# Optimization experiments

Measured on AMD Instinct MI355X. Metric: run time of the kernel, lower is better.

Reference implementation:

```python
import jax, jax.numpy as jnp
import numpy as np

GROUPS = 8
EPS = 1e-5

def setup_inputs() -> dict:
    key = jax.random.key(0)
    ks = jax.random.split(key, 5)
    B, C, H, W = 4, 256, 64, 64
    x = jax.random.normal(ks[0], (B, C, H, W), dtype=jnp.float32)
    gn_weight = jnp.ones((C,), dtype=jnp.float32)
    gn_bias = jnp.zeros((C,), dtype=jnp.float32)
    qkv_w = jax.random.normal(ks[1], (3 * C, C), dtype=jnp.float32) * (1.0 / np.sqrt(C))
    qkv_b = jax.random.normal(ks[2], (3 * C,), dtype=jnp.float32) * 0.02
    proj_w = jax.random.normal(ks[3], (C, C), dtype=jnp.float32) * (1.0 / np.sqrt(C))
    proj_b = jax.random.normal(ks[4], (C,), dtype=jnp.float32) * 0.02
    return {"x": x, "gn_weight": gn_weight, "gn_bias": gn_bias,
            "qkv_w": qkv_w, "qkv_b": qkv_b, "proj_w": proj_w, "proj_b": proj_b}

def _group_norm(x, weight, bias):
    B, C, H, W = x.shape
    xg = x.reshape(B, GROUPS, C // GROUPS, H, W)
    mean = jnp.mean(xg, axis=(2, 3, 4), keepdims=True)
    var = jnp.var(xg, axis=(2, 3, 4), keepdims=True)
    xn = ((xg - mean) * jax.lax.rsqrt(var + EPS)).reshape(B, C, H, W)
    return xn * weight[None, :, None, None] + bias[None, :, None, None]

def reference(x, gn_weight, gn_bias, qkv_w, qkv_b, proj_w, proj_b):
    B, C, H, W = x.shape
    N = H * W
    h = _group_norm(x, gn_weight, gn_bias)            # [B,C,H,W]
    hf = h.reshape(B, C, N)                           # [B,C,N]
    # 1x1 conv == channel matmul
    qkv = jnp.einsum('oc,bcn->bon', qkv_w, hf) + qkv_b[None, :, None]  # [B,3C,N]
    q, k, v = jnp.split(qkv, 3, axis=1)               # each [B,C,N]
    scale = 1.0 / jnp.sqrt(jnp.float32(C))
    attn = jax.nn.softmax(jnp.einsum('bcn,bcm->bnm', q, k) * scale, axis=-1)  # [B,N,N]
    o = jnp.einsum('bnm,bcm->bcn', attn, v)           # [B,C,N]
    o = jnp.einsum('oc,bcn->bon', proj_w, o) + proj_b[None, :, None]
    return x + o.reshape(B, C, H, W)
```

## Files before the change

### kernel.cpp

```cpp
#include <hip/hip_runtime.h>
#include <math.h>


#define BATCH 4
#define CH 256
#define NSP 4096
#define NGRP 8
#define CPG 32

typedef __attribute__((ext_vector_type(8))) short bf16x8;
typedef __attribute__((ext_vector_type(4))) float f32x4;

__device__ __forceinline__ unsigned short f2bf(float f) {
  union { float f; unsigned u; } v; v.f = f;
  unsigned r = v.u + 0x7FFF + ((v.u >> 16) & 1);
  return (unsigned short)(r >> 16);
}

__device__ __forceinline__ void gload_lds16(const void* g, void* l) {
  __builtin_amdgcn_global_load_lds(
      (const __attribute__((address_space(1))) unsigned int*)g,
      (__attribute__((address_space(3))) unsigned int*)l, 16, 0, 0);
}

__global__ __launch_bounds__(256) void gn_part_k(const float* __restrict__ x,
                                                 float* __restrict__ gpart) {
  const int bid = blockIdx.x;
  const int bg = bid >> 3, sl = bid & 7;
  const float4* p = (const float4*)(x + (size_t)bg * CPG * NSP + (size_t)sl * (CPG * NSP / 8));
  const int t = threadIdx.x;
  float s1 = 0.f, s2 = 0.f;
#pragma unroll
  for (int i = 0; i < 16; ++i) {
    float4 v = p[t + i * 256];
    s1 += v.x + v.y + v.z + v.w;
    s2 += v.x * v.x + v.y * v.y + v.z * v.z + v.w * v.w;
  }
  __shared__ float r1[256], r2[256];
  r1[t] = s1; r2[t] = s2;
  __syncthreads();
  for (int off = 128; off > 0; off >>= 1) {
    if (t < off) { r1[t] += r1[t + off]; r2[t] += r2[t + off]; }
    __syncthreads();
  }
  if (t == 0) { gpart[bid * 2] = r1[0]; gpart[bid * 2 + 1] = r2[0]; }
}

__global__ __launch_bounds__(256) void fold_k(const float* __restrict__ gn_w,
                                              const float* __restrict__ gn_b,
                                              const float* __restrict__ qkv_w,
                                              const float* __restrict__ qkv_b,
                                              const float* __restrict__ proj_w,
                                              const float* __restrict__ gpart,
                                              float* __restrict__ ascale,
                                              float* __restrict__ bias2,
                                              unsigned short* __restrict__ wb,
                                              unsigned short* __restrict__ pwb) {
  const int b = blockIdx.x;
  const int t = threadIdx.x;
  __shared__ float bb[CH];
  {
    const int c = t;
    const int g = c >> 5;
    float s1 = 0.f, s2 = 0.f;
#pragma unroll
    for (int s = 0; s < 8; ++s) {
      s1 += gpart[((b * NGRP + g) * 8 + s) * 2];
      s2 += gpart[((b * NGRP + g) * 8 + s) * 2 + 1];
    }
    const float inv = 1.f / (float)(CPG * NSP);
    const float mean = s1 * inv;
    const float var = s2 * inv - mean * mean;
    const float rstd = rsqrtf(var + 1e-5f);
    const float a = rstd * gn_w[c];
    ascale[b * CH + c] = a;
    bb[c] = gn_b[c] - mean * a;
  }
  __syncthreads();
  for (int o = t; o < 3 * CH; o += 256) {
    const float* wrow = qkv_w + (size_t)o * CH;
    float acc = qkv_b[o];
    for (int c = 0; c < CH; ++c) acc += wrow[c] * bb[c];
    if (o < CH) acc *= 0.0625f;
    bias2[b * 3 * CH + o] = acc;
  }
  for (int idx = t; idx < 192 * CH; idx += 256) {
    const int row = b * 192 + (idx >> 8);
    const int c = idx & 255;
    float w = qkv_w[(size_t)row * CH + c];
    if (row < CH) w *= 0.0625f;
    wb[(size_t)row * CH + c] = f2bf(w);
  }
  for (int idx = t; idx < 64 * CH; idx += 256) {
    const int row = b * 64 + (idx >> 8);
    const int c = idx & 255;
    pwb[(size_t)row * CH + c] = f2bf(proj_w[(size_t)row * CH + c]);
  }
}

__global__ __launch_bounds__(256) void xt_k(const float* __restrict__ x,
                                            const float* __restrict__ ascale,
                                            unsigned short* __restrict__ xbT) {
  const int b = blockIdx.z, cb = blockIdx.y * 64, nb = blockIdx.x * 64;
  const int t = threadIdx.x;
  __shared__ float Ls[64][68];
  for (int i = 0; i < 4; ++i) {
    const int idx = t + i * 256;
    const int c = idx >> 4, n4 = (idx & 15) << 2;
    const float a = ascale[b * CH + cb + c];
    const float4 v = *(const float4*)(x + ((size_t)(b * CH + cb + c)) * NSP + nb + n4);
    Ls[c][n4] = v.x * a; Ls[c][n4 + 1] = v.y * a;
    Ls[c][n4 + 2] = v.z * a; Ls[c][n4 + 3] = v.w * a;
  }
  __syncthreads();
  {
    const int n = t >> 2, cg = (t & 3) << 4;
    unsigned int pk[8];
#pragma unroll
    for (int j = 0; j < 8; ++j) {
      const unsigned short l16 = f2bf(Ls[cg + 2 * j][n]);
      const unsigned short h16 = f2bf(Ls[cg + 2 * j + 1][n]);
      pk[j] = (unsigned)l16 | ((unsigned)h16 << 16);
    }
    unsigned short* dst = xbT + ((size_t)(b * NSP) + nb + n) * CH + cb + cg;
    *(uint4*)dst = *(uint4*)&pk[0];
    *(uint4*)(dst + 8) = *(uint4*)&pk[4];
  }
}

__global__ __launch_bounds__(256) void qkv_mfma_k(const unsigned short* __restrict__ wb,
                                                  const unsigned short* __restrict__ xbT,
                                                  const float* __restrict__ bias2,
                                                  unsigned short* __restrict__ qT,
                                                  unsigned short* __restrict__ kT,
                                                  unsigned short* __restrict__ vN) {
  const int b = blockIdx.z, ob = blockIdx.y * 64, nb = blockIdx.x * 64;
  const int t = threadIdx.x;
  __shared__ short Ws[64][264];
  __shared__ short Xs[64][264];
  for (int i = 0; i < 8; ++i) {
    const int idx = t + i * 256;
    const int row = idx >> 5, u = (idx & 31) << 3;
    *(float4*)&Ws[row][u] = *(const float4*)(wb + ((size_t)(ob + row)) * CH + u);
    *(float4*)&Xs[row][u] = *(const float4*)(xbT + ((size_t)(b * NSP) + nb + row) * CH + u);
  }
  __syncthreads();
  const int lane = t & 63, wave = t >> 6, lo = lane & 15, hi = lane >> 4;
  const f32x4 zero = {0.f, 0.f, 0.f, 0.f};
  f32x4 acc[4] = {zero, zero, zero, zero};
#pragma unroll
  for (int ks = 0; ks < 8; ++ks) {
    const bf16x8 a = *(const bf16x8*)&Ws[wave * 16 + lo][ks * 32 + hi * 8];
#pragma unroll
    for (int nt = 0; nt < 4; ++nt) {
      const bf16x8 xv = *(const bf16x8*)&Xs[nt * 16 + lo][ks * 32 + hi * 8];
      acc[nt] = __builtin_amdgcn_mfma_f32_16x16x32_bf16(a, xv, acc[nt], 0, 0, 0);
    }
  }
#pragma unroll
  for (int nt = 0; nt < 4; ++nt) {
#pragma unroll
    for (int r = 0; r < 4; ++r) {
      const int o = ob + wave * 16 + hi * 4 + r;
      const int n = nb + nt * 16 + lo;
      const float v = acc[nt][r] + bias2[b * 3 * CH + o];
      if (o < CH)            qT[((size_t)(b * NSP) + n) * CH + o] = f2bf(v);
      else if (o < 2 * CH)   kT[((size_t)(b * NSP) + n) * CH + (o - CH)] = f2bf(v);
      else                   vN[((size_t)(b * CH) + (o - 2 * CH)) * NSP + n] = f2bf(v);
    }
  }
}

__global__ __launch_bounds__(512, 2) void attn_mfma_k(const unsigned short* __restrict__ qT,
                                                      const unsigned short* __restrict__ kT,
                                                      const unsigned short* __restrict__ vN,
                                                      unsigned short* __restrict__ oTb) {
  const int bid = blockIdx.x;
  const int L = (bid & 7) * 32 + (bid >> 3);
  const int b = L >> 6;
  const int qb = (L & 63) * 64;

  const int t = threadIdx.x;
  const int wid = t >> 6, lane = t & 63, lo = lane & 15, hi = lane >> 4;
  const int pair = wid >> 1, wip = wid & 1;

  __shared__ __align__(16) char smem[142336];
  short* Psw = (short*)(smem + 131072) + wid * 16 * 40;
  float* sM = (float*)(smem + 141312);
  float* sL = sM + 128;

  const unsigned short* kTb = kT + (size_t)b * NSP * CH;
  const unsigned short* vNb = vN + (size_t)b * CH * NSP;

  const int qrow = qb + pair * 16 + lo;
  bf16x8 qreg[8];
#pragma unroll
  for (int ks = 0; ks < 8; ++ks)
    qreg[ks] = *(const bf16x8*)(qT + ((size_t)(b * NSP) + qrow) * CH + ks * 32 + hi * 8);

  float mrun[4] = {-INFINITY, -INFINITY, -INFINITY, -INFINITY};
  float lrun[4] = {0.f, 0.f, 0.f, 0.f};
  const f32x4 zero = {0.f, 0.f, 0.f, 0.f};
  f32x4 oacc[16];
#pragma unroll
  for (int i = 0; i < 16; ++i) oacc[i] = zero;

  const int wbase = (t & ~63);

#define STAGE(KT_, BUF_)                                                        \
  {                                                                             \
    _Pragma("unroll")                                                           \
    for (int i_ = 0; i_ < 4; ++i_) {                                            \
      const int idx_ = t + i_ * 512;                                           \
      const int row_ = idx_ >> 5;                                              \
      const int cb_ = (idx_ & 31) << 4;                                        \
      const int scb_ = cb_ ^ ((row_ & 7) << 4);                                \
      gload_lds16(kTb + ((size_t)((KT_) + row_)) * CH + (scb_ >> 1),           \
                  smem + (BUF_)*32768 + ((wbase + i_ * 512) << 4));            \
    }                                                                           \
    _Pragma("unroll")                                                           \
    for (int i_ = 0; i_ < 4; ++i_) {                                            \
      const int idx_ = t + i_ * 512;                                           \
      const int row_ = idx_ >> 3;                                              \
      const int cb_ = (idx_ & 7) << 4;                                         \
      const int scb_ = cb_ ^ ((row_ & 7) << 4);                                \
      gload_lds16(vNb + (size_t)row_ * NSP + (KT_) + (scb_ >> 1),              \
                  smem + 65536 + (BUF_)*32768 + ((wbase + i_ * 512) << 4));    \
    }                                                                           \
  }

  STAGE(0, 0);
  __syncthreads();

  for (int tt = 0; tt < NSP / 64; ++tt) {
    const int cur = tt & 1;
    if (tt + 1 < NSP / 64) STAGE((tt + 1) * 64, cur ^ 1);

    f32x4 s[2] = {zero, zero};
    __builtin_amdgcn_s_setprio(1);
#pragma unroll
    for (int ks = 0; ks < 8; ++ks) {
#pragma unroll
      for (int mt = 0; mt < 2; ++mt) {
        const int row = wip * 32 + mt * 16 + lo;
        const int cb = (ks * 64 + hi * 16) ^ ((row & 7) << 4);
        const bf16x8 kv = *(const bf16x8*)(smem + cur * 32768 + row * 512 + cb);
        s[mt] = __builtin_amdgcn_mfma_f32_16x16x32_bf16(qreg[ks], kv, s[mt], 0, 0, 0);
      }
    }
    __builtin_amdgcn_s_setprio(0);

    float mx[4];
#pragma unroll
    for (int r = 0; r < 4; ++r) {
      float m_ = fmaxf(s[0][r], s[1][r]);
      m_ = fmaxf(m_, __shfl_xor(m_, 1));
      m_ = fmaxf(m_, __shfl_xor(m_, 2));
      m_ = fmaxf(m_, __shfl_xor(m_, 4));
      m_ = fmaxf(m_, __shfl_xor(m_, 8));
      mx[r] = m_;
    }
    const bool grow = (mx[0] > mrun[0] + 8.f) | (mx[1] > mrun[1] + 8.f) |
                      (mx[2] > mrun[2] + 8.f) | (mx[3] > mrun[3] + 8.f);
    if (__any(grow)) {
#pragma unroll
      for (int r = 0; r < 4; ++r) {
        const float mm = fmaxf(mx[r], mrun[r]);
        const float al = __expf(mrun[r] - mm);
        mrun[r] = mm;
        lrun[r] *= al;
#pragma unroll
        for (int ct = 0; ct < 16; ++ct) oacc[ct][r] *= al;
      }
    }
#pragma unroll
    for (int r = 0; r < 4; ++r) {
      const float mm = mrun[r];
      const float p0 = __expf(s[0][r] - mm);
      const float p1 = __expf(s[1][r] - mm);
      Psw[(hi * 4 + r) * 40 + lo] = (short)f2bf(p0);
      Psw[(hi * 4 + r) * 40 + 16 + lo] = (short)f2bf(p1);
      float ps = p0 + p1;
      ps += __shfl_xor(ps, 1);
      ps += __shfl_xor(ps, 2);
      ps += __shfl_xor(ps, 4);
      ps += __shfl_xor(ps, 8);
      lrun[r] += ps;
    }

    const bf16x8 pa = *(const bf16x8*)&Psw[lo * 40 + hi * 8];
    __builtin_amdgcn_s_setprio(1);
#pragma unroll
    for (int ct = 0; ct < 16; ++ct) {
      const int c = ct * 16 + lo;
      const int cb = (wip * 64 + hi * 16) ^ ((c & 7) << 4);
      const bf16x8 vv = *(const bf16x8*)(smem + 65536 + cur * 32768 + c * 128 + cb);
      oacc[ct] = __builtin_amdgcn_mfma_f32_16x16x32_bf16(pa, vv, oacc[ct], 0, 0, 0);
    }
    __builtin_amdgcn_s_setprio(0);

    __syncthreads();
  }

  if (lo == 0) {
#pragma unroll
    for (int r = 0; r < 4; ++r) {
      sM[(pair * 2 + wip) * 16 + hi * 4 + r] = mrun[r];
      sL[(pair * 2 + wip) * 16 + hi * 4 + r] = lrun[r];
    }
  }
  __syncthreads();
  float e[4], ltot[4];
#pragma unroll
  for (int r = 0; r < 4; ++r) {
    const float mo = sM[(pair * 2 + (wip ^ 1)) * 16 + hi * 4 + r];
    const float lo_ = sL[(pair * 2 + (wip ^ 1)) * 16 + hi * 4 + r];
    const float mm = fmaxf(mrun[r], mo);
    e[r] = __expf(mrun[r] - mm);
    const float eo = __expf(mo - mm);
    ltot[r] = e[r] * lrun[r] + eo * lo_;
#pragma unroll
    for (int ct = 0; ct < 16; ++ct) oacc[ct][r] *= e[r];
  }
  float* Obuf = (float*)smem;
  if (wip == 1) {
#pragma unroll
    for (int ct = 0; ct < 16; ++ct)
#pragma unroll
      for (int r = 0; r < 4; ++r)
        Obuf[(pair * 16 + hi * 4 + r) * 260 + ct * 16 + lo] = oacc[ct][r];
  }
  __syncthreads();
  if (wip == 0) {
#pragma unroll
    for (int r = 0; r < 4; ++r) {
      const float li = 1.f / ltot[r];
      const int n = qb + pair * 16 + hi * 4 + r;
#pragma unroll
      for (int ct = 0; ct < 16; ++ct) {
        const float v = (oacc[ct][r] + Obuf[(pair * 16 + hi * 4 + r) * 260 + ct * 16 + lo]) * li;
        oTb[((size_t)(b * NSP) + n) * CH + ct * 16 + lo] = f2bf(v);
      }
    }
  }
#undef STAGE
}

__global__ __launch_bounds__(256) void proj_mfma_k(const unsigned short* __restrict__ pwb,
                                                   const unsigned short* __restrict__ oTb,
                                                   const float* __restrict__ proj_b,
                                                   const float* __restrict__ x,
                                                   float* __restrict__ out) {
  const int b = blockIdx.z, ob = blockIdx.y * 64, nb = blockIdx.x * 64;
  const int t = threadIdx.x;
  __shared__ short Ws[64][264];
  __shared__ short Os[64][264];
  for (int i = 0; i < 8; ++i) {
    const int idx = t + i * 256;
    const int row = idx >> 5, u = (idx & 31) << 3;
    *(float4*)&Ws[row][u] = *(const float4*)(pwb + ((size_t)(ob + row)) * CH + u);
    *(float4*)&Os[row][u] = *(const float4*)(oTb + ((size_t)(b * NSP) + nb + row) * CH + u);
  }
  __syncthreads();
  const int lane = t & 63, wave = t >> 6, lo = lane & 15, hi = lane >> 4;
  const f32x4 zero = {0.f, 0.f, 0.f, 0.f};
  f32x4 acc[4] = {zero, zero, zero, zero};
#pragma unroll
  for (int ks = 0; ks < 8; ++ks) {
    const bf16x8 a = *(const bf16x8*)&Ws[wave * 16 + lo][ks * 32 + hi * 8];
#pragma unroll
    for (int nt = 0; nt < 4; ++nt) {
      const bf16x8 ov = *(const bf16x8*)&Os[nt * 16 + lo][ks * 32 + hi * 8];
      acc[nt] = __builtin_amdgcn_mfma_f32_16x16x32_bf16(a, ov, acc[nt], 0, 0, 0);
    }
  }
#pragma unroll
  for (int nt = 0; nt < 4; ++nt) {
#pragma unroll
    for (int r = 0; r < 4; ++r) {
      const int o = ob + wave * 16 + hi * 4 + r;
      const int n = nb + nt * 16 + lo;
      const size_t off = ((size_t)(b * CH + o)) * NSP + n;
      out[off] = acc[nt][r] + proj_b[o] + x[off];
    }
  }
}

extern "C" void kernel_launch(void* const* d_in, const int* in_sizes, int n_in,
                              void* d_out, int out_size, void* d_ws, size_t ws_size,
                              hipStream_t stream) {
  const float* x      = (const float*)d_in[0];
  const float* gn_w   = (const float*)d_in[1];
  const float* gn_b   = (const float*)d_in[2];
  const float* qkv_w  = (const float*)d_in[3];
  const float* qkv_b  = (const float*)d_in[4];
  const float* proj_w = (const float*)d_in[5];
  const float* proj_b = (const float*)d_in[6];
  float* out = (float*)d_out;

  char* w = (char*)d_ws;
  unsigned short* qT  = (unsigned short*)w; w += (size_t)BATCH * NSP * CH * 2;
  unsigned short* kT  = (unsigned short*)w; w += (size_t)BATCH * NSP * CH * 2;
  unsigned short* vN  = (unsigned short*)w; w += (size_t)BATCH * NSP * CH * 2;
  unsigned short* xbT = (unsigned short*)w; w += (size_t)BATCH * NSP * CH * 2;
  unsigned short* oTb = (unsigned short*)w; w += (size_t)BATCH * NSP * CH * 2;
  unsigned short* wb  = (unsigned short*)w; w += (size_t)3 * CH * CH * 2;
  unsigned short* pwb = (unsigned short*)w; w += (size_t)CH * CH * 2;
  float* gpart  = (float*)w; w += 512 * 4;
  float* ascale = (float*)w; w += BATCH * CH * 4;
  float* bias2  = (float*)w; w += BATCH * 3 * CH * 4;

  gn_part_k<<<256, 256, 0, stream>>>(x, gpart);
  fold_k<<<BATCH, 256, 0, stream>>>(gn_w, gn_b, qkv_w, qkv_b, proj_w, gpart,
                                    ascale, bias2, wb, pwb);
  xt_k<<<dim3(NSP / 64, CH / 64, BATCH), 256, 0, stream>>>(x, ascale, xbT);
  qkv_mfma_k<<<dim3(NSP / 64, 3 * CH / 64, BATCH), 256, 0, stream>>>(wb, xbT, bias2, qT, kT, vN);
  attn_mfma_k<<<256, 512, 0, stream>>>(qT, kT, vN, oTb);
  proj_mfma_k<<<dim3(NSP / 64, CH / 64, BATCH), 256, 0, stream>>>(pwb, oTb, proj_b, x, out);
}
```

Before: 330.7 us.

## Rewrite attention kernel with 32x32x16 MFMA, register-resident P, and 4-wave blocks

The attention kernel moves from 16x16x32 MFMAs with 8 waves to 32x32x16 MFMAs with 4 waves, each wave holding 32 query rows. QK^T is computed transposed, so the softmax row max and sum need only one cross-half shuffle. P is repacked into the B operand through lane shuffles instead of a round trip through LDS. The next tile's prefetch is issued after the softmax rather than before QK. This cuts LDS traffic, shuffles and the per-row softmax bookkeeping, at the cost of more registers per thread and fewer waves available to hide latency.

```diff
diff --git a/kernel.cpp b/kernel.cpp
--- a/kernel.cpp
+++ b/kernel.cpp
@@ -10,11 +10,16 @@
 
 typedef __attribute__((ext_vector_type(8))) short bf16x8;
 typedef __attribute__((ext_vector_type(4))) float f32x4;
+typedef __attribute__((ext_vector_type(16))) float f32x16;
 
 __device__ __forceinline__ unsigned short f2bf(float f) {
   union { float f; unsigned u; } v; v.f = f;
   unsigned r = v.u + 0x7FFF + ((v.u >> 16) & 1);
   return (unsigned short)(r >> 16);
+}
+
+__device__ __forceinline__ unsigned pk2bf(float a, float b) {
+  return (unsigned)f2bf(a) | ((unsigned)f2bf(b) << 16);
 }
 
 __device__ __forceinline__ void gload_lds16(const void* g, void* l) {
@@ -171,7 +176,7 @@
   }
 }
 
-__global__ __launch_bounds__(512, 2) void attn_mfma_k(const unsigned short* __restrict__ qT,
+__global__ __launch_bounds__(256, 1) void attn_mfma_k(const unsigned short* __restrict__ qT,
                                                       const unsigned short* __restrict__ kT,
                                                       const unsigned short* __restrict__ vN,
                                                       unsigned short* __restrict__ oTb) {
@@ -181,51 +186,54 @@
   const int qb = (L & 63) * 64;
 
   const int t = threadIdx.x;
-  const int wid = t >> 6, lane = t & 63, lo = lane & 15, hi = lane >> 4;
-  const int pair = wid >> 1, wip = wid & 1;
-
-  __shared__ __align__(16) char smem[142336];
-  short* Psw = (short*)(smem + 131072) + wid * 16 * 40;
-  float* sM = (float*)(smem + 141312);
-  float* sL = sM + 128;
+  const int wid = t >> 6, lane = t & 63;
+  const int cl = lane & 31, h = lane >> 5;
+  const int qg = wid >> 1, mh = wid & 1;
+
+  __shared__ __align__(16) char smem[132096];
+  float* sM = (float*)(smem + 131072);
+  float* sL = (float*)(smem + 131584);
 
   const unsigned short* kTb = kT + (size_t)b * NSP * CH;
   const unsigned short* vNb = vN + (size_t)b * CH * NSP;
 
-  const int qrow = qb + pair * 16 + lo;
-  bf16x8 qreg[8];
-#pragma unroll
-  for (int ks = 0; ks < 8; ++ks)
-    qreg[ks] = *(const bf16x8*)(qT + ((size_t)(b * NSP) + qrow) * CH + ks * 32 + hi * 8);
-
-  float mrun[4] = {-INFINITY, -INFINITY, -INFINITY, -INFINITY};
-  float lrun[4] = {0.f, 0.f, 0.f, 0.f};
-  const f32x4 zero = {0.f, 0.f, 0.f, 0.f};
-  f32x4 oacc[16];
-#pragma unroll
-  for (int i = 0; i < 16; ++i) oacc[i] = zero;
+  bf16x8 qreg[16];
+  {
+    const unsigned short* qp = qT + ((size_t)(b * NSP) + qb + qg * 32 + cl) * CH + h * 8;
+#pragma unroll
+    for (int ks = 0; ks < 16; ++ks) qreg[ks] = *(const bf16x8*)(qp + ks * 16);
+  }
+
+  const f32x16 z16 = {0.f,0.f,0.f,0.f,0.f,0.f,0.f,0.f,0.f,0.f,0.f,0.f,0.f,0.f,0.f,0.f};
+  float mrun = -INFINITY, lrun = 0.f;
+  f32x16 oacc[8];
+#pragma unroll
+  for (int i = 0; i < 8; ++i) oacc[i] = z16;
 
   const int wbase = (t & ~63);
+  const int rowbase = (mh * 32 + cl) * 512;
+  const int rswz = (cl & 7) << 4;
 
 #define STAGE(KT_, BUF_)                                                        \
   {                                                                             \
     _Pragma("unroll")                                                           \
-    for (int i_ = 0; i_ < 4; ++i_) {                                            \
-      const int idx_ = t + i_ * 512;                                           \
-      const int row_ = idx_ >> 5;                                              \
-      const int cb_ = (idx_ & 31) << 4;                                        \
-      const int scb_ = cb_ ^ ((row_ & 7) << 4);                                \
-      gload_lds16(kTb + ((size_t)((KT_) + row_)) * CH + (scb_ >> 1),           \
-                  smem + (BUF_)*32768 + ((wbase + i_ * 512) << 4));            \
+    for (int i_ = 0; i_ < 8; ++i_) {                                            \
+      const int idx_ = t + i_ * 256;                                            \
+      const int row_ = idx_ >> 5;                                               \
+      const int cby_ = (idx_ & 31) << 4;                                        \
+      const int scb_ = cby_ ^ ((row_ & 7) << 4);                                \
+      gload_lds16(kTb + ((size_t)((KT_) + row_)) * CH + (scb_ >> 1),            \
+                  smem + (BUF_) * 32768 + ((wbase + i_ * 256) << 4));           \
     }                                                                           \
     _Pragma("unroll")                                                           \
-    for (int i_ = 0; i_ < 4; ++i_) {                                            \
-      const int idx_ = t + i_ * 512;                                           \
-      const int row_ = idx_ >> 3;                                              \
-      const int cb_ = (idx_ & 7) << 4;                                         \
-      const int scb_ = cb_ ^ ((row_ & 7) << 4);                                \
-      gload_lds16(vNb + (size_t)row_ * NSP + (KT_) + (scb_ >> 1),              \
-                  smem + 65536 + (BUF_)*32768 + ((wbase + i_ * 512) << 4));    \
+    for (int i_ = 0; i_ < 8; ++i_) {                                            \
+      const int idx_ = t + i_ * 256;                                            \
+      const int rv_ = idx_ >> 4;                                                \
+      const int inner_ = (idx_ & 15) << 4;                                      \
+      const int ch_ = rv_ * 2 + (inner_ >> 7);                                  \
+      const int mby_ = (inner_ & 127) ^ ((rv_ & 7) << 4);                       \
+      gload_lds16(vNb + (size_t)ch_ * NSP + (KT_) + (mby_ >> 1),                \
+                  smem + 65536 + (BUF_) * 32768 + ((wbase + i_ * 256) << 4));   \
     }                                                                           \
   }
 
@@ -234,112 +242,111 @@
 
   for (int tt = 0; tt < NSP / 64; ++tt) {
     const int cur = tt & 1;
+    const char* Kb = smem + cur * 32768 + rowbase;
+    const char* Vb = smem + 65536 + cur * 32768;
+
+    f32x16 s0 = z16, s1 = z16;
+    __builtin_amdgcn_s_setprio(1);
+#pragma unroll
+    for (int ks = 0; ks < 16; ks += 2) {
+      const bf16x8 a0 = *(const bf16x8*)(Kb + ((ks * 32 + h * 16) ^ rswz));
+      const bf16x8 a1 = *(const bf16x8*)(Kb + (((ks + 1) * 32 + h * 16) ^ rswz));
+      s0 = __builtin_amdgcn_mfma_f32_32x32x16_bf16(a0, qreg[ks], s0, 0, 0, 0);
+      s1 = __builtin_amdgcn_mfma_f32_32x32x16_bf16(a1, qreg[ks + 1], s1, 0, 0, 0);
+    }
+    __builtin_amdgcn_s_setprio(0);
+    const f32x16 s = s0 + s1;
+
+    float mx = s[0];
+#pragma unroll
+    for (int r = 1; r < 16; ++r) mx = fmaxf(mx, s[r]);
+    mx = fmaxf(mx, __shfl_xor(mx, 32));
+    if (__any(mx > mrun + 8.f)) {
+      const float mm = fmaxf(mx, mrun);
+      const float al = __expf(mrun - mm);
+      mrun = mm;
+      lrun *= al;
+#pragma unroll
+      for (int cf = 0; cf < 8; ++cf) oacc[cf] *= al;
+    }
+    float p[16];
+    float ps = 0.f;
+#pragma unroll
+    for (int r = 0; r < 16; ++r) { p[r] = __expf(s[r] - mrun); ps += p[r]; }
+    ps += __shfl_xor(ps, 32);
+    lrun += ps;
+
+    const unsigned w0 = pk2bf(p[0], p[1]),   w1 = pk2bf(p[2], p[3]);
+    const unsigned w2 = pk2bf(p[4], p[5]),   w3 = pk2bf(p[6], p[7]);
+    const unsigned w4 = pk2bf(p[8], p[9]),   w5 = pk2bf(p[10], p[11]);
+    const unsigned w6 = pk2bf(p[12], p[13]), w7 = pk2bf(p[14], p[15]);
+    const unsigned e0 = __shfl_xor(h ? w0 : w2, 32);
+    const unsigned e1 = __shfl_xor(h ? w1 : w3, 32);
+    const unsigned e2 = __shfl_xor(h ? w4 : w6, 32);
+    const unsigned e3 = __shfl_xor(h ? w5 : w7, 32);
+    union { bf16x8 v; unsigned u[4]; } B0, B1;
+    B0.u[0] = h ? e0 : w0;  B0.u[1] = h ? e1 : w1;
+    B0.u[2] = h ? w2 : e0;  B0.u[3] = h ? w3 : e1;
+    B1.u[0] = h ? e2 : w4;  B1.u[1] = h ? e3 : w5;
+    B1.u[2] = h ? w6 : e2;  B1.u[3] = h ? w7 : e3;
+
     if (tt + 1 < NSP / 64) STAGE((tt + 1) * 64, cur ^ 1);
 
-    f32x4 s[2] = {zero, zero};
     __builtin_amdgcn_s_setprio(1);
 #pragma unroll
-    for (int ks = 0; ks < 8; ++ks) {
-#pragma unroll
-      for (int mt = 0; mt < 2; ++mt) {
-        const int row = wip * 32 + mt * 16 + lo;
-        const int cb = (ks * 64 + hi * 16) ^ ((row & 7) << 4);
-        const bf16x8 kv = *(const bf16x8*)(smem + cur * 32768 + row * 512 + cb);
-        s[mt] = __builtin_amdgcn_mfma_f32_16x16x32_bf16(qreg[ks], kv, s[mt], 0, 0, 0);
-      }
+    for (int cf = 0; cf < 8; ++cf) {
+      const int c = cf * 32 + cl;
+      const char* vrow = Vb + (c >> 1) * 256 + (c & 1) * 128;
+      const int sw = ((c >> 1) & 7) << 4;
+      const bf16x8 va0 = *(const bf16x8*)(vrow + ((mh * 64 + h * 16) ^ sw));
+      const bf16x8 va1 = *(const bf16x8*)(vrow + ((mh * 64 + 32 + h * 16) ^ sw));
+      oacc[cf] = __builtin_amdgcn_mfma_f32_32x32x16_bf16(va0, B0.v, oacc[cf], 0, 0, 0);
+      oacc[cf] = __builtin_amdgcn_mfma_f32_32x32x16_bf16(va1, B1.v, oacc[cf], 0, 0, 0);
     }
     __builtin_amdgcn_s_setprio(0);
 
-    float mx[4];
-#pragma unroll
-    for (int r = 0; r < 4; ++r) {
-      float m_ = fmaxf(s[0][r], s[1][r]);
-      m_ = fmaxf(m_, __shfl_xor(m_, 1));
-      m_ = fmaxf(m_, __shfl_xor(m_, 2));
-      m_ = fmaxf(m_, __shfl_xor(m_, 4));
-      m_ = fmaxf(m_, __shfl_xor(m_, 8));
-      mx[r] = m_;
-    }
-    const bool grow = (mx[0] > mrun[0] + 8.f) | (mx[1] > mrun[1] + 8.f) |
-                      (mx[2] > mrun[2] + 8.f) | (mx[3] > mrun[3] + 8.f);
-    if (__any(grow)) {
-#pragma unroll
-      for (int r = 0; r < 4; ++r) {
-        const float mm = fmaxf(mx[r], mrun[r]);
-        const float al = __expf(mrun[r] - mm);
-        mrun[r] = mm;
-        lrun[r] *= al;
-#pragma unroll
-        for (int ct = 0; ct < 16; ++ct) oacc[ct][r] *= al;
-      }
-    }
-#pragma unroll
-    for (int r = 0; r < 4; ++r) {
-      const float mm = mrun[r];
-      const float p0 = __expf(s[0][r] - mm);
-      const float p1 = __expf(s[1][r] - mm);
-      Psw[(hi * 4 + r) * 40 + lo] = (short)f2bf(p0);
-      Psw[(hi * 4 + r) * 40 + 16 + lo] = (short)f2bf(p1);
-      float ps = p0 + p1;
-      ps += __shfl_xor(ps, 1);
-      ps += __shfl_xor(ps, 2);
-      ps += __shfl_xor(ps, 4);
-      ps += __shfl_xor(ps, 8);
-      lrun[r] += ps;
-    }
-
-    const bf16x8 pa = *(const bf16x8*)&Psw[lo * 40 + hi * 8];
-    __builtin_amdgcn_s_setprio(1);
-#pragma unroll
-    for (int ct = 0; ct < 16; ++ct) {
-      const int c = ct * 16 + lo;
-      const int cb = (wip * 64 + hi * 16) ^ ((c & 7) << 4);
-      const bf16x8 vv = *(const bf16x8*)(smem + 65536 + cur * 32768 + c * 128 + cb);
-      oacc[ct] = __builtin_amdgcn_mfma_f32_16x16x32_bf16(pa, vv, oacc[ct], 0, 0, 0);
-    }
-    __builtin_amdgcn_s_setprio(0);
-
     __syncthreads();
   }
 
-  if (lo == 0) {
-#pragma unroll
-    for (int r = 0; r < 4; ++r) {
-      sM[(pair * 2 + wip) * 16 + hi * 4 + r] = mrun[r];
-      sL[(pair * 2 + wip) * 16 + hi * 4 + r] = lrun[r];
-    }
-  }
-  __syncthreads();
-  float e[4], ltot[4];
-#pragma unroll
-  for (int r = 0; r < 4; ++r) {
-    const float mo = sM[(pair * 2 + (wip ^ 1)) * 16 + hi * 4 + r];
-    const float lo_ = sL[(pair * 2 + (wip ^ 1)) * 16 + hi * 4 + r];
-    const float mm = fmaxf(mrun[r], mo);
-    e[r] = __expf(mrun[r] - mm);
-    const float eo = __expf(mo - mm);
-    ltot[r] = e[r] * lrun[r] + eo * lo_;
-#pragma unroll
-    for (int ct = 0; ct < 16; ++ct) oacc[ct][r] *= e[r];
-  }
+  if (h == 0) {
+    sM[(qg * 2 + mh) * 32 + cl] = mrun;
+    sL[(qg * 2 + mh) * 32 + cl] = lrun;
+  }
+  __syncthreads();
+  const float mo = sM[(qg * 2 + (mh ^ 1)) * 32 + cl];
+  const float lo_ = sL[(qg * 2 + (mh ^ 1)) * 32 + cl];
+  const float mm2 = fmaxf(mrun, mo);
+  const float e = __expf(mrun - mm2);
+  const float ltot = e * lrun + __expf(mo - mm2) * lo_;
+#pragma unroll
+  for (int cf = 0; cf < 8; ++cf) oacc[cf] *= e;
+
   float* Obuf = (float*)smem;
-  if (wip == 1) {
-#pragma unroll
-    for (int ct = 0; ct < 16; ++ct)
-#pragma unroll
-      for (int r = 0; r < 4; ++r)
-        Obuf[(pair * 16 + hi * 4 + r) * 260 + ct * 16 + lo] = oacc[ct][r];
-  }
-  __syncthreads();
-  if (wip == 0) {
-#pragma unroll
-    for (int r = 0; r < 4; ++r) {
-      const float li = 1.f / ltot[r];
-      const int n = qb + pair * 16 + hi * 4 + r;
-#pragma unroll
-      for (int ct = 0; ct < 16; ++ct) {
-        const float v = (oacc[ct][r] + Obuf[(pair * 16 + hi * 4 + r) * 260 + ct * 16 + lo]) * li;
-        oTb[((size_t)(b * NSP) + n) * CH + ct * 16 + lo] = f2bf(v);
+  float* Ob = Obuf + (qg * 32 + cl) * 264;
+  if (mh == 1) {
+#pragma unroll
+    for (int cf = 0; cf < 8; ++cf)
+#pragma unroll
+      for (int r = 0; r < 16; ++r)
+        Ob[cf * 32 + (r & 3) + 8 * (r >> 2) + 4 * h] = oacc[cf][r];
+  }
+  __syncthreads();
+  if (mh == 0) {
+    const float inv = 1.f / ltot;
+    unsigned short* dst = oTb + ((size_t)(b * NSP) + qb + qg * 32 + cl) * CH;
+#pragma unroll
+    for (int cf = 0; cf < 8; ++cf) {
+#pragma unroll
+      for (int g = 0; g < 4; ++g) {
+        const int c0 = cf * 32 + 8 * g + 4 * h;
+        const float v0 = (oacc[cf][4 * g + 0] + Ob[c0 + 0]) * inv;
+        const float v1 = (oacc[cf][4 * g + 1] + Ob[c0 + 1]) * inv;
+        const float v2 = (oacc[cf][4 * g + 2] + Ob[c0 + 2]) * inv;
+        const float v3 = (oacc[cf][4 * g + 3] + Ob[c0 + 3]) * inv;
+        uint2 pkd;
+        pkd.x = pk2bf(v0, v1);
+        pkd.y = pk2bf(v2, v3);
+        *(uint2*)(dst + c0) = pkd;
       }
     }
   }
@@ -415,6 +422,6 @@
                                     ascale, bias2, wb, pwb);
   xt_k<<<dim3(NSP / 64, CH / 64, BATCH), 256, 0, stream>>>(x, ascale, xbT);
   qkv_mfma_k<<<dim3(NSP / 64, 3 * CH / 64, BATCH), 256, 0, stream>>>(wb, xbT, bias2, qT, kT, vN);
-  attn_mfma_k<<<256, 512, 0, stream>>>(qT, kT, vN, oTb);
+  attn_mfma_k<<<256, 256, 0, stream>>>(qT, kT, vN, oTb);
   proj_mfma_k<<<dim3(NSP / 64, CH / 64, BATCH), 256, 0, stream>>>(pwb, oTb, proj_b, x, out);
 }
```

New measurement: 302.9 us. 8.4% less time.
